# Kernel tuning notes

Measured on AMD Instinct MI355X. Metric: run time of the kernel, lower is better.

Reference implementation:

```python
import jax, jax.numpy as jnp
import numpy as np

B, T, E, H, O = 64, 512, 512, 512, 512

def setup_inputs() -> dict:
    key = jax.random.key(0)
    k1, k2, k3, k4, k5 = jax.random.split(key, 5)
    s1 = 1.0 / np.sqrt(E + H)
    s2 = 1.0 / np.sqrt(H)
    return {
        "x": jax.random.normal(k1, (B, T, E), dtype=jnp.float32),
        "W1": jax.random.uniform(k2, (H, E + H), dtype=jnp.float32, minval=-s1, maxval=s1),
        "b1": jax.random.uniform(k3, (H,), dtype=jnp.float32, minval=-s1, maxval=s1),
        "W2": jax.random.uniform(k4, (O, H), dtype=jnp.float32, minval=-s2, maxval=s2),
        "b2": jax.random.uniform(k5, (O,), dtype=jnp.float32, minval=-s2, maxval=s2),
    }

def reference(x, W1, b1, W2, b2):
    b = x.shape[0]
    h0 = jnp.zeros((b, x.shape[2]), dtype=x.dtype)

    def step(hidden, xt):
        inp = jnp.concatenate([xt, hidden], axis=1)          # [b, e+h]
        hidden = jax.nn.relu(inp @ W1.T + b1)                # [b, h]
        out = hidden @ W2.T + b2                             # [b, o]
        return hidden, out

    # scan over time: x -> [t, b, e]
    h_final, outs = jax.lax.scan(step, h0, jnp.swapaxes(x, 0, 1))
    return jnp.swapaxes(outs, 0, 1), h_final
```

## Files before the change

kernel.cpp:

```cpp
#include <hip/hip_runtime.h>
#include <cstddef>

#define T_STEPS 512
#define BATCH   64
#define EDIM    512
#define HDIM    512
#define ODIM    512

#define HPAD    520
#define W_ELEMS (32 * 4 * 64 * 8)
#define H_ELEMS (16 * HPAD)
#define SMEM_BYTES ((W_ELEMS + H_ELEMS) * 2)

typedef __bf16 bf16;
typedef __bf16 bf16x8 __attribute__((ext_vector_type(8)));
typedef float  f32x4  __attribute__((ext_vector_type(4)));

template <typename XT>
__global__ __launch_bounds__(256) void gemm_mfma_kernel(
    const XT* __restrict__ X, int ldx,
    const float* __restrict__ W, int ldw, int kw0,
    const float* __restrict__ bias,
    float* __restrict__ C, int ldc, int K)
{
  __shared__ __align__(16) bf16 Asm[8 * 64 * 8];
  __shared__ __align__(16) bf16 Bsm[8 * 64 * 8];

  const int tid  = threadIdx.x;
  const int row0 = blockIdx.x * 128;
  const int col0 = blockIdx.y * 128;
  const int w    = tid >> 6, lane = tid & 63;
  const int q    = lane >> 4, nl = lane & 15;
  const int wm   = w >> 1, wn = w & 1;

  f32x4 acc[4][4] = {};

  for (int k0 = 0; k0 < K; k0 += 32) {
#pragma unroll
    for (int rep = 0; rep < 2; ++rep) {
      int idx = tid + rep * 256;
      int mt = idx >> 6, l2 = idx & 63;
      const XT* src = X + (size_t)(row0 + mt * 16 + (l2 & 15)) * ldx
                        + k0 + (l2 >> 4) * 8;
      bf16x8 v;
#pragma unroll
      for (int u = 0; u < 8; ++u) v[u] = (bf16)(float)src[u];
      *(bf16x8*)&Asm[(size_t)idx * 8] = v;
    }
#pragma unroll
    for (int rep = 0; rep < 2; ++rep) {
      int idx = tid + rep * 256;
      int nt = idx >> 6, l2 = idx & 63;
      const float* src = W + (size_t)(col0 + nt * 16 + (l2 & 15)) * ldw
                           + kw0 + k0 + (l2 >> 4) * 8;
      bf16x8 v;
#pragma unroll
      for (int u = 0; u < 8; ++u) v[u] = (bf16)src[u];
      *(bf16x8*)&Bsm[(size_t)idx * 8] = v;
    }
    __syncthreads();

    bf16x8 a[4], b[4];
#pragma unroll
    for (int i = 0; i < 4; ++i)
      a[i] = *(bf16x8*)&Asm[(size_t)((wm * 4 + i) * 64 + lane) * 8];
#pragma unroll
    for (int j = 0; j < 4; ++j)
      b[j] = *(bf16x8*)&Bsm[(size_t)((wn * 4 + j) * 64 + lane) * 8];
#pragma unroll
    for (int i = 0; i < 4; ++i)
#pragma unroll
      for (int j = 0; j < 4; ++j)
        acc[i][j] = __builtin_amdgcn_mfma_f32_16x16x32_bf16(a[i], b[j], acc[i][j], 0, 0, 0);
    __syncthreads();
  }

#pragma unroll
  for (int i = 0; i < 4; ++i)
#pragma unroll
    for (int j = 0; j < 4; ++j) {
      int colg = col0 + wn * 64 + j * 16 + nl;
#pragma unroll
      for (int r = 0; r < 4; ++r) {
        size_t rowg = (size_t)(row0 + wm * 64 + i * 16 + q * 4 + r);
        C[rowg * ldc + colg] = acc[i][j][r] + bias[colg];
      }
    }
}

__global__ __launch_bounds__(512, 2) void scan_big_kernel(
    const float* __restrict__ A,
    const float* __restrict__ W1,
    bf16* __restrict__ Hbf)
{
  extern __shared__ __align__(16) bf16 smem[];
  bf16* Wlds = smem;
  bf16* hsm  = smem + W_ELEMS;

  const int tid  = threadIdx.x;
  const int c    = blockIdx.x;
  const int w    = tid >> 6, lane = tid & 63;
  const int q    = lane >> 4, nl = lane & 15;
  const int rb0  = c * 16;

  for (int idx = tid; idx < 32 * 4 * 64; idx += 512) {
    int l  = idx & 63;
    int kt = (idx >> 6) & 3;
    int tg = idx >> 8;
    int n  = tg * 16 + (l & 15);
    int k  = kt * 32 + (l >> 4) * 8;
    const float* src = W1 + (size_t)n * (EDIM + HDIM) + EDIM + k;
    bf16x8 v;
#pragma unroll
    for (int u = 0; u < 8; ++u) v[u] = (bf16)src[u];
    *(bf16x8*)&Wlds[(size_t)idx * 8] = v;
  }

  bf16x8 Wreg[4][12];
#pragma unroll
  for (int i = 0; i < 4; ++i) {
    int n = w * 64 + i * 16 + nl;
    const float* wrow = W1 + (size_t)n * (EDIM + HDIM) + EDIM;
#pragma unroll
    for (int kt2 = 0; kt2 < 12; ++kt2) {
      const float* src = wrow + (kt2 + 4) * 32 + q * 8;
      bf16x8 v;
#pragma unroll
      for (int u = 0; u < 8; ++u) v[u] = (bf16)src[u];
      Wreg[i][kt2] = v;
    }
  }
  __syncthreads();

  float An[4][4];
#pragma unroll
  for (int i = 0; i < 4; ++i)
#pragma unroll
    for (int r = 0; r < 4; ++r)
      An[i][r] = A[((size_t)(rb0 + q * 4 + r) * T_STEPS + 0) * HDIM
                   + w * 64 + i * 16 + nl];

  f32x4 acc[4];

  for (int t = 0; t < T_STEPS; ++t) {
    if (t > 0) {
      int m = tid >> 5, j = tid & 31;
      bf16x8 h0 = *(bf16x8*)&hsm[m * HPAD + j * 16];
      bf16x8 h1 = *(bf16x8*)&hsm[m * HPAD + j * 16 + 8];
      bf16* dst = Hbf + ((size_t)(rb0 + m) * T_STEPS + (t - 1)) * HDIM + j * 16;
      *(bf16x8*)dst       = h0;
      *(bf16x8*)(dst + 8) = h1;
    }

#pragma unroll
    for (int i = 0; i < 4; ++i)
#pragma unroll
      for (int r = 0; r < 4; ++r) acc[i][r] = An[i][r];

    {
      int tn = (t + 1 < T_STEPS) ? t + 1 : 0;
#pragma unroll
      for (int i = 0; i < 4; ++i)
#pragma unroll
        for (int r = 0; r < 4; ++r)
          An[i][r] = A[((size_t)(rb0 + q * 4 + r) * T_STEPS + tn) * HDIM
                       + w * 64 + i * 16 + nl];
    }

    if (t > 0) {
#pragma unroll
      for (int kt = 0; kt < 16; ++kt) {
        bf16x8 af = *(bf16x8*)&hsm[nl * HPAD + kt * 32 + q * 8];
        if (kt < 4) {
#pragma unroll
          for (int i = 0; i < 4; ++i) {
            bf16x8 b = *(bf16x8*)&Wlds[(size_t)(((w * 4 + i) * 4 + kt) * 64 + lane) * 8];
            acc[i] = __builtin_amdgcn_mfma_f32_16x16x32_bf16(af, b, acc[i], 0, 0, 0);
          }
        } else {
#pragma unroll
          for (int i = 0; i < 4; ++i)
            acc[i] = __builtin_amdgcn_mfma_f32_16x16x32_bf16(af, Wreg[i][kt - 4], acc[i], 0, 0, 0);
        }
      }
    }

    __syncthreads();

#pragma unroll
    for (int i = 0; i < 4; ++i)
#pragma unroll
      for (int r = 0; r < 4; ++r) {
        float v = acc[i][r] > 0.0f ? acc[i][r] : 0.0f;
        hsm[(q * 4 + r) * HPAD + w * 64 + i * 16 + nl] = (bf16)v;
      }

    __syncthreads();
  }

  {
    int m = tid >> 5, j = tid & 31;
    bf16x8 h0 = *(bf16x8*)&hsm[m * HPAD + j * 16];
    bf16x8 h1 = *(bf16x8*)&hsm[m * HPAD + j * 16 + 8];
    bf16* dst = Hbf + ((size_t)(rb0 + m) * T_STEPS + (T_STEPS - 1)) * HDIM + j * 16;
    *(bf16x8*)dst       = h0;
    *(bf16x8*)(dst + 8) = h1;
  }
}

#define HALF 256
__global__ __launch_bounds__(512) void scan_fallback_kernel(
    const float* __restrict__ A,
    const float* __restrict__ W1,
    bf16* __restrict__ Hbf,
    int* __restrict__ flags)
{
  __shared__ __align__(16) bf16 WldsF[16 * 2 * 64 * 8];
  __shared__ __align__(16) bf16 hsmF[16 * HPAD];

  const int tid   = threadIdx.x;
  const int bid   = blockIdx.x;
  const int c     = bid >> 1;
  const int s     = bid & 1;
  const int col0  = s * HALF;
  const int pcol0 = (1 - s) * HALF;
  const int rb0   = c * 16;
  const int w     = tid >> 6, lane = tid & 63;
  const int q     = lane >> 4, nl = lane & 15;

  for (int idx = tid; idx < 16 * 2 * 64; idx += 512) {
    int l  = idx & 63;
    int kt = (idx >> 6) & 1;
    int tg = idx >> 7;
    int n  = col0 + tg * 16 + (l & 15);
    int k  = kt * 32 + (l >> 4) * 8;
    const float* src = W1 + (size_t)n * (EDIM + HDIM) + EDIM + k;
    bf16x8 v;
#pragma unroll
    for (int u = 0; u < 8; ++u) v[u] = (bf16)src[u];
    *(bf16x8*)&WldsF[(size_t)idx * 8] = v;
  }

  bf16x8 Wreg[2][14];
#pragma unroll
  for (int i = 0; i < 2; ++i) {
    int n = col0 + w * 32 + i * 16 + nl;
    const float* wrow = W1 + (size_t)n * (EDIM + HDIM) + EDIM;
#pragma unroll
    for (int kt2 = 0; kt2 < 14; ++kt2) {
      const float* src = wrow + (kt2 + 2) * 32 + q * 8;
      bf16x8 v;
#pragma unroll
      for (int u = 0; u < 8; ++u) v[u] = (bf16)src[u];
      Wreg[i][kt2] = v;
    }
  }
  __syncthreads();

  int* myflag = flags + (c * 2 + s) * 32;
  int* paflag = flags + (c * 2 + (1 - s)) * 32;

  float Ac[2][4], An[2][4];
#pragma unroll
  for (int i = 0; i < 2; ++i)
#pragma unroll
    for (int r = 0; r < 4; ++r)
      Ac[i][r] = A[((size_t)(rb0 + q * 4 + r) * T_STEPS + 0) * HDIM
                   + col0 + w * 32 + i * 16 + nl];

  f32x4 acc[2];

  for (int t = 0; t < T_STEPS; ++t) {
    if (t > 0) {
      if (tid == 0) {
        while (__hip_atomic_load(paflag, __ATOMIC_RELAXED,
                                 __HIP_MEMORY_SCOPE_AGENT) < t) {}
      }
      __syncthreads();
      __threadfence();
      int m = tid >> 5, j = tid & 31;
      bf16x8 hv = *(const bf16x8*)(
          Hbf + ((size_t)(rb0 + m) * T_STEPS + (t - 1)) * HDIM + pcol0 + j * 8);
      *(bf16x8*)&hsmF[m * HPAD + pcol0 + j * 8] = hv;
    }

#pragma unroll
    for (int i = 0; i < 2; ++i)
#pragma unroll
      for (int r = 0; r < 4; ++r) acc[i][r] = Ac[i][r];

    {
      int tn = (t + 1 < T_STEPS) ? t + 1 : 0;
#pragma unroll
      for (int i = 0; i < 2; ++i)
#pragma unroll
        for (int r = 0; r < 4; ++r)
          An[i][r] = A[((size_t)(rb0 + q * 4 + r) * T_STEPS + tn) * HDIM
                       + col0 + w * 32 + i * 16 + nl];
    }

    if (t > 0) {
      __syncthreads();
#pragma unroll
      for (int kt = 0; kt < 16; ++kt) {
        bf16x8 af = *(bf16x8*)&hsmF[nl * HPAD + kt * 32 + q * 8];
        if (kt < 2) {
#pragma unroll
          for (int i = 0; i < 2; ++i) {
            bf16x8 b = *(bf16x8*)&WldsF[(size_t)(((w * 2 + i) * 2 + kt) * 64 + lane) * 8];
            acc[i] = __builtin_amdgcn_mfma_f32_16x16x32_bf16(af, b, acc[i], 0, 0, 0);
          }
        } else {
#pragma unroll
          for (int i = 0; i < 2; ++i)
            acc[i] = __builtin_amdgcn_mfma_f32_16x16x32_bf16(af, Wreg[i][kt - 2], acc[i], 0, 0, 0);
        }
      }
    }

    __syncthreads();

#pragma unroll
    for (int i = 0; i < 2; ++i)
#pragma unroll
      for (int r = 0; r < 4; ++r) {
        float v = acc[i][r] > 0.0f ? acc[i][r] : 0.0f;
        int colg = col0 + w * 32 + i * 16 + nl;
        hsmF[(q * 4 + r) * HPAD + colg] = (bf16)v;
        Hbf[((size_t)(rb0 + q * 4 + r) * T_STEPS + t) * HDIM + colg] = (bf16)v;
      }

#pragma unroll
    for (int i = 0; i < 2; ++i)
#pragma unroll
      for (int r = 0; r < 4; ++r) Ac[i][r] = An[i][r];

    __syncthreads();
    if (tid == 0) {
      __threadfence();
      __hip_atomic_fetch_add(myflag, 1, __ATOMIC_RELAXED,
                             __HIP_MEMORY_SCOPE_AGENT);
    }
  }
}

__global__ __launch_bounds__(256) void copy_hfinal_kernel(
    const bf16* __restrict__ Hbf, float* __restrict__ out)
{
  int i = blockIdx.x * blockDim.x + threadIdx.x;
  int b = i / HDIM, n = i % HDIM;
  out[i] = (float)Hbf[((size_t)b * T_STEPS + (T_STEPS - 1)) * HDIM + n];
}

extern "C" void kernel_launch(void* const* d_in, const int* in_sizes, int n_in,
                              void* d_out, int out_size, void* d_ws, size_t ws_size,
                              hipStream_t stream) {
  const float* x  = (const float*)d_in[0];
  const float* W1 = (const float*)d_in[1];
  const float* b1 = (const float*)d_in[2];
  const float* W2 = (const float*)d_in[3];
  const float* b2 = (const float*)d_in[4];

  float* out = (float*)d_out;
  float* A   = out;

  bf16* Hbf  = (bf16*)d_ws;
  int* flags = (int*)((char*)d_ws + (size_t)BATCH * T_STEPS * HDIM * 2);

  hipMemsetAsync(flags, 0, 8 * 32 * sizeof(int), stream);

  {
    dim3 grid(BATCH * T_STEPS / 128, HDIM / 128);
    gemm_mfma_kernel<float><<<grid, 256, 0, stream>>>(
        x, EDIM, W1, EDIM + HDIM, 0, b1, A, HDIM, EDIM);
  }

  hipError_t e = hipFuncSetAttribute(
      reinterpret_cast<const void*>(scan_big_kernel),
      hipFuncAttributeMaxDynamicSharedMemorySize, SMEM_BYTES);
  if (e == hipSuccess) {
    scan_big_kernel<<<4, 512, SMEM_BYTES, stream>>>(A, W1, Hbf);
  } else {
    scan_fallback_kernel<<<8, 512, 0, stream>>>(A, W1, Hbf, flags);
  }

  {
    dim3 grid(BATCH * T_STEPS / 128, ODIM / 128);
    gemm_mfma_kernel<bf16><<<grid, 256, 0, stream>>>(
        Hbf, HDIM, W2, HDIM, 0, b2, out, ODIM, HDIM);
  }

  copy_hfinal_kernel<<<(BATCH * HDIM) / 256, 256, 0, stream>>>(
      Hbf, out + (size_t)BATCH * T_STEPS * ODIM);
}
```

Baseline: 1.398 ms.

## Split recurrent scan across paired blocks with register-resident weights and time-major A

Replaces the single-block-per-batch-chunk scan, which used large dynamic LDS, with a split kernel. Two blocks share each batch chunk, each owning half the hidden columns and exchanging halves through global memory with flag spin-waits. Each block keeps its full W1 hidden slice in registers and overlaps its local-half MFMAs with the partner-half load. The input projection GEMM now writes A in time-major layout so the per-step prefetch is a contiguous vector load. The grid launches 16 blocks and only 8 do work, apparently to place partners on separate CUs or XCDs. In exchange, cross-block synchronization latency is added on every step.

```diff
diff --git a/kernel.cpp b/kernel.cpp
--- a/kernel.cpp
+++ b/kernel.cpp
@@ -8,15 +8,14 @@
 #define ODIM    512
 
 #define HPAD    520
-#define W_ELEMS (32 * 4 * 64 * 8)
-#define H_ELEMS (16 * HPAD)
-#define SMEM_BYTES ((W_ELEMS + H_ELEMS) * 2)
+#define HALF    256
 
 typedef __bf16 bf16;
+typedef __bf16 bf16x4 __attribute__((ext_vector_type(4)));
 typedef __bf16 bf16x8 __attribute__((ext_vector_type(8)));
 typedef float  f32x4  __attribute__((ext_vector_type(4)));
 
-template <typename XT>
+template <typename XT, bool REMAP>
 __global__ __launch_bounds__(256) void gemm_mfma_kernel(
     const XT* __restrict__ X, int ldx,
     const float* __restrict__ W, int ldw, int kw0,
@@ -83,257 +82,112 @@
 #pragma unroll
       for (int r = 0; r < 4; ++r) {
         size_t rowg = (size_t)(row0 + wm * 64 + i * 16 + q * 4 + r);
-        C[rowg * ldc + colg] = acc[i][j][r] + bias[colg];
-      }
-    }
-}
-
-__global__ __launch_bounds__(512, 2) void scan_big_kernel(
-    const float* __restrict__ A,
-    const float* __restrict__ W1,
-    bf16* __restrict__ Hbf)
-{
-  extern __shared__ __align__(16) bf16 smem[];
-  bf16* Wlds = smem;
-  bf16* hsm  = smem + W_ELEMS;
-
-  const int tid  = threadIdx.x;
-  const int c    = blockIdx.x;
-  const int w    = tid >> 6, lane = tid & 63;
-  const int q    = lane >> 4, nl = lane & 15;
-  const int rb0  = c * 16;
-
-  for (int idx = tid; idx < 32 * 4 * 64; idx += 512) {
-    int l  = idx & 63;
-    int kt = (idx >> 6) & 3;
-    int tg = idx >> 8;
-    int n  = tg * 16 + (l & 15);
-    int k  = kt * 32 + (l >> 4) * 8;
-    const float* src = W1 + (size_t)n * (EDIM + HDIM) + EDIM + k;
-    bf16x8 v;
-#pragma unroll
-    for (int u = 0; u < 8; ++u) v[u] = (bf16)src[u];
-    *(bf16x8*)&Wlds[(size_t)idx * 8] = v;
-  }
-
-  bf16x8 Wreg[4][12];
-#pragma unroll
-  for (int i = 0; i < 4; ++i) {
-    int n = w * 64 + i * 16 + nl;
-    const float* wrow = W1 + (size_t)n * (EDIM + HDIM) + EDIM;
-#pragma unroll
-    for (int kt2 = 0; kt2 < 12; ++kt2) {
-      const float* src = wrow + (kt2 + 4) * 32 + q * 8;
-      bf16x8 v;
-#pragma unroll
-      for (int u = 0; u < 8; ++u) v[u] = (bf16)src[u];
-      Wreg[i][kt2] = v;
-    }
-  }
-  __syncthreads();
-
-  float An[4][4];
-#pragma unroll
-  for (int i = 0; i < 4; ++i)
-#pragma unroll
-    for (int r = 0; r < 4; ++r)
-      An[i][r] = A[((size_t)(rb0 + q * 4 + r) * T_STEPS + 0) * HDIM
-                   + w * 64 + i * 16 + nl];
-
-  f32x4 acc[4];
-
-  for (int t = 0; t < T_STEPS; ++t) {
-    if (t > 0) {
-      int m = tid >> 5, j = tid & 31;
-      bf16x8 h0 = *(bf16x8*)&hsm[m * HPAD + j * 16];
-      bf16x8 h1 = *(bf16x8*)&hsm[m * HPAD + j * 16 + 8];
-      bf16* dst = Hbf + ((size_t)(rb0 + m) * T_STEPS + (t - 1)) * HDIM + j * 16;
-      *(bf16x8*)dst       = h0;
-      *(bf16x8*)(dst + 8) = h1;
-    }
-
-#pragma unroll
-    for (int i = 0; i < 4; ++i)
-#pragma unroll
-      for (int r = 0; r < 4; ++r) acc[i][r] = An[i][r];
-
-    {
-      int tn = (t + 1 < T_STEPS) ? t + 1 : 0;
-#pragma unroll
-      for (int i = 0; i < 4; ++i)
-#pragma unroll
-        for (int r = 0; r < 4; ++r)
-          An[i][r] = A[((size_t)(rb0 + q * 4 + r) * T_STEPS + tn) * HDIM
-                       + w * 64 + i * 16 + nl];
-    }
-
-    if (t > 0) {
-#pragma unroll
-      for (int kt = 0; kt < 16; ++kt) {
-        bf16x8 af = *(bf16x8*)&hsm[nl * HPAD + kt * 32 + q * 8];
-        if (kt < 4) {
-#pragma unroll
-          for (int i = 0; i < 4; ++i) {
-            bf16x8 b = *(bf16x8*)&Wlds[(size_t)(((w * 4 + i) * 4 + kt) * 64 + lane) * 8];
-            acc[i] = __builtin_amdgcn_mfma_f32_16x16x32_bf16(af, b, acc[i], 0, 0, 0);
-          }
-        } else {
-#pragma unroll
-          for (int i = 0; i < 4; ++i)
-            acc[i] = __builtin_amdgcn_mfma_f32_16x16x32_bf16(af, Wreg[i][kt - 4], acc[i], 0, 0, 0);
-        }
-      }
-    }
-
-    __syncthreads();
-
-#pragma unroll
-    for (int i = 0; i < 4; ++i)
-#pragma unroll
-      for (int r = 0; r < 4; ++r) {
-        float v = acc[i][r] > 0.0f ? acc[i][r] : 0.0f;
-        hsm[(q * 4 + r) * HPAD + w * 64 + i * 16 + nl] = (bf16)v;
-      }
-
-    __syncthreads();
-  }
-
-  {
-    int m = tid >> 5, j = tid & 31;
-    bf16x8 h0 = *(bf16x8*)&hsm[m * HPAD + j * 16];
-    bf16x8 h1 = *(bf16x8*)&hsm[m * HPAD + j * 16 + 8];
-    bf16* dst = Hbf + ((size_t)(rb0 + m) * T_STEPS + (T_STEPS - 1)) * HDIM + j * 16;
-    *(bf16x8*)dst       = h0;
-    *(bf16x8*)(dst + 8) = h1;
-  }
-}
-
-#define HALF 256
-__global__ __launch_bounds__(512) void scan_fallback_kernel(
+        size_t crow = REMAP ? (((rowg & (T_STEPS - 1)) << 6) | (rowg >> 9)) : rowg;
+        C[crow * ldc + colg] = acc[i][j][r] + bias[colg];
+      }
+    }
+}
+
+__global__ __launch_bounds__(512, 2) void scan_split_kernel(
     const float* __restrict__ A,
     const float* __restrict__ W1,
     bf16* __restrict__ Hbf,
     int* __restrict__ flags)
 {
-  __shared__ __align__(16) bf16 WldsF[16 * 2 * 64 * 8];
-  __shared__ __align__(16) bf16 hsmF[16 * HPAD];
+  const int bid = blockIdx.x;
+  int c, s;
+  if (bid < 4)                   { c = bid;     s = 0; }
+  else if (bid >= 8 && bid < 12) { c = bid - 8; s = 1; }
+  else return;
+
+  __shared__ __align__(16) bf16 hsm[16 * HPAD];
 
   const int tid   = threadIdx.x;
-  const int bid   = blockIdx.x;
-  const int c     = bid >> 1;
-  const int s     = bid & 1;
   const int col0  = s * HALF;
   const int pcol0 = (1 - s) * HALF;
   const int rb0   = c * 16;
   const int w     = tid >> 6, lane = tid & 63;
   const int q     = lane >> 4, nl = lane & 15;
-
-  for (int idx = tid; idx < 16 * 2 * 64; idx += 512) {
-    int l  = idx & 63;
-    int kt = (idx >> 6) & 1;
-    int tg = idx >> 7;
-    int n  = col0 + tg * 16 + (l & 15);
-    int k  = kt * 32 + (l >> 4) * 8;
-    const float* src = W1 + (size_t)n * (EDIM + HDIM) + EDIM + k;
-    bf16x8 v;
-#pragma unroll
-    for (int u = 0; u < 8; ++u) v[u] = (bf16)src[u];
-    *(bf16x8*)&WldsF[(size_t)idx * 8] = v;
-  }
-
-  bf16x8 Wreg[2][14];
-#pragma unroll
-  for (int i = 0; i < 2; ++i) {
-    int n = col0 + w * 32 + i * 16 + nl;
-    const float* wrow = W1 + (size_t)n * (EDIM + HDIM) + EDIM;
-#pragma unroll
-    for (int kt2 = 0; kt2 < 14; ++kt2) {
-      const float* src = wrow + (kt2 + 2) * 32 + q * 8;
-      bf16x8 v;
-#pragma unroll
-      for (int u = 0; u < 8; ++u) v[u] = (bf16)src[u];
-      Wreg[i][kt2] = v;
-    }
-  }
-  __syncthreads();
+  const int n0    = col0 + w * 32;
+  const int m_ex  = tid >> 5;
+  const int j_ex  = tid & 31;
 
   int* myflag = flags + (c * 2 + s) * 32;
   int* paflag = flags + (c * 2 + (1 - s)) * 32;
 
-  float Ac[2][4], An[2][4];
-#pragma unroll
-  for (int i = 0; i < 2; ++i)
-#pragma unroll
-    for (int r = 0; r < 4; ++r)
-      Ac[i][r] = A[((size_t)(rb0 + q * 4 + r) * T_STEPS + 0) * HDIM
-                   + col0 + w * 32 + i * 16 + nl];
+  bf16x8 Wreg[2][16];
+#pragma unroll
+  for (int i = 0; i < 2; ++i) {
+    const float* wrow = W1 + (size_t)(n0 + i * 16 + nl) * (EDIM + HDIM) + EDIM + q * 8;
+#pragma unroll
+    for (int j = 0; j < 16; ++j) {
+      int kg = (j < 8) ? (s * 8 + j) : ((1 - s) * 8 + (j - 8));
+      const float* src = wrow + kg * 32;
+      bf16x8 v;
+#pragma unroll
+      for (int u = 0; u < 8; ++u) v[u] = (bf16)src[u];
+      Wreg[i][j] = v;
+    }
+  }
+
+  f32x4 An[2];
+  {
+    const float* ap = A + ((size_t)(rb0 + nl)) * HDIM + n0 + q * 4;
+    An[0] = *(const f32x4*)ap;
+    An[1] = *(const f32x4*)(ap + 16);
+  }
 
   f32x4 acc[2];
 
   for (int t = 0; t < T_STEPS; ++t) {
-    if (t > 0) {
-      if (tid == 0) {
-        while (__hip_atomic_load(paflag, __ATOMIC_RELAXED,
-                                 __HIP_MEMORY_SCOPE_AGENT) < t) {}
-      }
-      __syncthreads();
-      __threadfence();
-      int m = tid >> 5, j = tid & 31;
-      bf16x8 hv = *(const bf16x8*)(
-          Hbf + ((size_t)(rb0 + m) * T_STEPS + (t - 1)) * HDIM + pcol0 + j * 8);
-      *(bf16x8*)&hsmF[m * HPAD + pcol0 + j * 8] = hv;
-    }
-
-#pragma unroll
-    for (int i = 0; i < 2; ++i)
-#pragma unroll
-      for (int r = 0; r < 4; ++r) acc[i][r] = Ac[i][r];
-
+    acc[0] = An[0];
+    acc[1] = An[1];
     {
       int tn = (t + 1 < T_STEPS) ? t + 1 : 0;
-#pragma unroll
-      for (int i = 0; i < 2; ++i)
-#pragma unroll
-        for (int r = 0; r < 4; ++r)
-          An[i][r] = A[((size_t)(rb0 + q * 4 + r) * T_STEPS + tn) * HDIM
-                       + col0 + w * 32 + i * 16 + nl];
-    }
-
+      const float* ap = A + ((size_t)tn * BATCH + rb0 + nl) * HDIM + n0 + q * 4;
+      An[0] = *(const f32x4*)ap;
+      An[1] = *(const f32x4*)(ap + 16);
+    }
+
+    unsigned long long p0 = 0, p1 = 0;
     if (t > 0) {
+      while (__hip_atomic_load(paflag, __ATOMIC_RELAXED,
+                               __HIP_MEMORY_SCOPE_AGENT) < t) {}
+      unsigned long long* src = (unsigned long long*)(
+          Hbf + ((size_t)(rb0 + m_ex) * T_STEPS + (t - 1)) * HDIM + pcol0 + j_ex * 8);
+      p0 = __hip_atomic_load(src,     __ATOMIC_RELAXED, __HIP_MEMORY_SCOPE_AGENT);
+      p1 = __hip_atomic_load(src + 1, __ATOMIC_RELAXED, __HIP_MEMORY_SCOPE_AGENT);
+    }
+
+    if (t > 0) {
+#pragma unroll
+      for (int kk = 0; kk < 8; ++kk) {
+        bf16x8 af = *(bf16x8*)&hsm[nl * HPAD + col0 + kk * 32 + q * 8];
+        acc[0] = __builtin_amdgcn_mfma_f32_16x16x32_bf16(Wreg[0][kk], af, acc[0], 0, 0, 0);
+        acc[1] = __builtin_amdgcn_mfma_f32_16x16x32_bf16(Wreg[1][kk], af, acc[1], 0, 0, 0);
+      }
+      {
+        union { unsigned long long u[2]; bf16x8 v; } P;
+        P.u[0] = p0; P.u[1] = p1;
+        *(bf16x8*)&hsm[m_ex * HPAD + pcol0 + j_ex * 8] = P.v;
+      }
       __syncthreads();
 #pragma unroll
-      for (int kt = 0; kt < 16; ++kt) {
-        bf16x8 af = *(bf16x8*)&hsmF[nl * HPAD + kt * 32 + q * 8];
-        if (kt < 2) {
-#pragma unroll
-          for (int i = 0; i < 2; ++i) {
-            bf16x8 b = *(bf16x8*)&WldsF[(size_t)(((w * 2 + i) * 2 + kt) * 64 + lane) * 8];
-            acc[i] = __builtin_amdgcn_mfma_f32_16x16x32_bf16(af, b, acc[i], 0, 0, 0);
-          }
-        } else {
-#pragma unroll
-          for (int i = 0; i < 2; ++i)
-            acc[i] = __builtin_amdgcn_mfma_f32_16x16x32_bf16(af, Wreg[i][kt - 2], acc[i], 0, 0, 0);
-        }
-      }
-    }
-
-    __syncthreads();
-
-#pragma unroll
-    for (int i = 0; i < 2; ++i)
-#pragma unroll
-      for (int r = 0; r < 4; ++r) {
-        float v = acc[i][r] > 0.0f ? acc[i][r] : 0.0f;
-        int colg = col0 + w * 32 + i * 16 + nl;
-        hsmF[(q * 4 + r) * HPAD + colg] = (bf16)v;
-        Hbf[((size_t)(rb0 + q * 4 + r) * T_STEPS + t) * HDIM + colg] = (bf16)v;
-      }
-
-#pragma unroll
-    for (int i = 0; i < 2; ++i)
-#pragma unroll
-      for (int r = 0; r < 4; ++r) Ac[i][r] = An[i][r];
+      for (int kk = 0; kk < 8; ++kk) {
+        bf16x8 af = *(bf16x8*)&hsm[nl * HPAD + pcol0 + kk * 32 + q * 8];
+        acc[0] = __builtin_amdgcn_mfma_f32_16x16x32_bf16(Wreg[0][8 + kk], af, acc[0], 0, 0, 0);
+        acc[1] = __builtin_amdgcn_mfma_f32_16x16x32_bf16(Wreg[1][8 + kk], af, acc[1], 0, 0, 0);
+      }
+    }
+
+#pragma unroll
+    for (int i = 0; i < 2; ++i) {
+      bf16x4 hv;
+#pragma unroll
+      for (int r = 0; r < 4; ++r) hv[r] = (bf16)fmaxf(acc[i][r], 0.0f);
+      *(bf16x4*)&hsm[nl * HPAD + n0 + i * 16 + q * 4] = hv;
+      *(bf16x4*)(Hbf + ((size_t)(rb0 + nl) * T_STEPS + t) * HDIM + n0 + i * 16 + q * 4) = hv;
+    }
 
     __syncthreads();
     if (tid == 0) {
@@ -371,22 +225,15 @@
 
   {
     dim3 grid(BATCH * T_STEPS / 128, HDIM / 128);
-    gemm_mfma_kernel<float><<<grid, 256, 0, stream>>>(
+    gemm_mfma_kernel<float, true><<<grid, 256, 0, stream>>>(
         x, EDIM, W1, EDIM + HDIM, 0, b1, A, HDIM, EDIM);
   }
 
-  hipError_t e = hipFuncSetAttribute(
-      reinterpret_cast<const void*>(scan_big_kernel),
-      hipFuncAttributeMaxDynamicSharedMemorySize, SMEM_BYTES);
-  if (e == hipSuccess) {
-    scan_big_kernel<<<4, 512, SMEM_BYTES, stream>>>(A, W1, Hbf);
-  } else {
-    scan_fallback_kernel<<<8, 512, 0, stream>>>(A, W1, Hbf, flags);
-  }
+  scan_split_kernel<<<16, 512, 0, stream>>>(A, W1, Hbf, flags);
 
   {
     dim3 grid(BATCH * T_STEPS / 128, ODIM / 128);
-    gemm_mfma_kernel<bf16><<<grid, 256, 0, stream>>>(
+    gemm_mfma_kernel<bf16, false><<<grid, 256, 0, stream>>>(
         Hbf, HDIM, W2, HDIM, 0, b2, out, ODIM, HDIM);
   }
 
```

Result: slower. 1.574 ms (+12.6%).
